# Kernel tuning notes

Measured on AMD Instinct MI355X. Metric: run time of the kernel, lower is better.

Reference implementation:

```python
import jax, jax.numpy as jnp
import numpy as np

ST_HIDDEN = 128
ST_HEADS = 4
ST_LAYERS = 3
RES_SCALE = 1.0
DK = ST_HIDDEN // ST_HEADS


def build_3d_adj(spatial_ei, spatial_ea, n_nodes, window):
    # replicate spatial edges per time slice with node offset t*n_nodes
    offs = (jnp.arange(window) * n_nodes)[None, :, None]  # [1,W,1]
    all_sp_idx = (spatial_ei[:, None, :] + offs).reshape(2, -1)  # [2, W*E]
    all_sp_attr = jnp.tile(spatial_ea, (window, 1))  # [W*E, De]
    # temporal edges t -> t+1 for every node
    src = jnp.arange((window - 1) * n_nodes)
    temp_idx = jnp.stack([src, src + n_nodes], axis=0)  # [2, (W-1)*N]
    temp_attr = jnp.broadcast_to(spatial_ea.mean(axis=0, keepdims=True),
                                 (temp_idx.shape[1], spatial_ea.shape[1]))
    ei = jnp.concatenate([all_sp_idx, temp_idx], axis=1)
    ea = jnp.concatenate([all_sp_attr, temp_attr], axis=0)
    return ei, ea


def seg_softmax(logits, dst, num_nodes):
    # logits [E,H], segment softmax over dst (pyg_softmax)
    m = jax.ops.segment_max(logits, dst, num_segments=num_nodes)  # [N,H]
    ex = jnp.exp(logits - m[dst])
    s = jax.ops.segment_sum(ex, dst, num_segments=num_nodes)
    return ex / (s[dst] + 1e-16)


def layernorm(x, g, b, eps=1e-5):
    mu = x.mean(-1, keepdims=True)
    var = ((x - mu) ** 2).mean(-1, keepdims=True)
    return (x - mu) * jax.lax.rsqrt(var + eps) * g + b


def block(x, ei, ea, qw, qb, kw, kb, vw, vb, fw, fb, ow, ob, ln_g, ln_b):
    B, Nt, _ = x.shape
    H, dk = ST_HEADS, DK
    Q = (x @ qw + qb).reshape(B, Nt, H, dk)
    K = (x @ kw + kb).reshape(B, Nt, H, dk)
    V = (x @ vw + vb).reshape(B, Nt, H, dk)
    src, dst = ei[0], ei[1]
    q_e = Q[:, dst]  # [B,E,H,dk]
    k_e = K[:, src]
    v_e = V[:, src]
    film = ea @ fw + fb  # [E, 2*hidden]
    gamma, beta = jnp.split(film, 2, axis=-1)
    gamma = gamma.reshape(1, -1, H, dk)
    beta = beta.reshape(1, -1, H, dk)
    k_e = k_e * (1.0 + gamma) + beta
    logits = (q_e * k_e).sum(-1) / np.sqrt(dk).astype(np.float32)  # [B,E,H]
    att = jax.vmap(lambda l: seg_softmax(l, dst, Nt))(logits)
    msg = att[..., None] * v_e  # [B,E,H,dk]
    out = jnp.zeros((B, Nt, H, dk), x.dtype).at[:, dst].add(msg)
    y = out.reshape(B, Nt, H * dk) @ ow + ob
    return layernorm(x + y, ln_g, ln_b)


def setup_inputs() -> dict:
    key = jax.random.key(0)
    ks = jax.random.split(key, 12)
    B, W, N, Fin, E, De = 2, 16, 1000, 16, 16000, 8
    H, L = ST_HIDDEN, ST_LAYERS
    g = lambda k, s: jax.random.normal(k, s, jnp.float32) * 0.05
    return {
        "xw": jax.random.normal(ks[0], (B, W, N, Fin), jnp.float32),
        "spatial_ei": jax.random.randint(ks[1], (2, E), 0, N),
        "spatial_ea": jax.random.normal(ks[2], (E, De), jnp.float32),
        "in_w": g(ks[3], (Fin, H)), "in_b": jnp.zeros((H,), jnp.float32),
        "qw": g(ks[4], (L, H, H)), "qb": jnp.zeros((L, H), jnp.float32),
        "kw": g(ks[5], (L, H, H)), "kb": jnp.zeros((L, H), jnp.float32),
        "vw": g(ks[6], (L, H, H)), "vb": jnp.zeros((L, H), jnp.float32),
        "fw": g(ks[7], (L, De, 2 * H)), "fb": jnp.zeros((L, 2 * H), jnp.float32),
        "ow": g(ks[8], (L, H, H)), "ob": jnp.zeros((L, H), jnp.float32),
        "ln_g": jnp.ones((L, H), jnp.float32), "ln_b": jnp.zeros((L, H), jnp.float32),
        "head_w": g(ks[9], (H, 1)), "head_b": jnp.zeros((1,), jnp.float32),
    }


def reference(xw, spatial_ei, spatial_ea, in_w, in_b, qw, qb, kw, kb, vw, vb,
              fw, fb, ow, ob, ln_g, ln_b, head_w, head_b):
    B, W, N, Fin = xw.shape
    ei, ea = build_3d_adj(spatial_ei, spatial_ea, N, W)
    x = xw.reshape(B, W * N, Fin) @ in_w + in_b
    for l in range(ST_LAYERS):
        bx = block(x, ei, ea, qw[l], qb[l], kw[l], kb[l], vw[l], vb[l],
                   fw[l], fb[l], ow[l], ob[l], ln_g[l], ln_b[l])
        x = x + RES_SCALE * (bx - x)
    last = x.reshape(B, W, N, -1)[:, -1]  # [B,N,H]
    return jax.nn.softplus(last @ head_w + head_b).squeeze(-1)  # [B,N]
```

## Files before the change

### kernel.cpp

```cpp
#include <hip/hip_runtime.h>
#include <math.h>

constexpr int B    = 2;
constexpr int W    = 16;
constexpr int N    = 1000;
constexpr int FIN  = 16;
constexpr int E    = 16000;
constexpr int DE   = 8;
constexpr int H    = 128;
constexpr int L    = 3;
constexpr int WL   = 4;
constexpr int W0G  = 12;
constexpr int RPB  = WL * N;
constexpr int ROWS = B * RPB;
constexpr int NMAT = 12;
constexpr int NFILM = (E + 1 + 7) / 8;

__device__ __forceinline__ float dot4(float4 a, float4 b) {
  return a.x * b.x + a.y * b.y + a.z * b.z + a.w * b.w;
}
__device__ __forceinline__ float dpp_add_xor1(float x) {
  int y = __builtin_amdgcn_update_dpp(0, __float_as_int(x), 0xB1, 0xF, 0xF, true);
  return x + __int_as_float(y);
}
__device__ __forceinline__ float dpp_add_xor2(float x) {
  int y = __builtin_amdgcn_update_dpp(0, __float_as_int(x), 0x4E, 0xF, 0xF, true);
  return x + __int_as_float(y);
}
__device__ __forceinline__ float headSum32(float p) {
  p = dpp_add_xor1(p);
  p = dpp_add_xor2(p);
  p += __shfl_xor(p, 4);
  p += __shfl_xor(p, 8);
  p += __shfl_xor(p, 16);
  return p;
}

__global__ void k_prep(const int* __restrict__ ei, const float* __restrict__ ea,
                       const float* __restrict__ qw, const float* __restrict__ kw,
                       const float* __restrict__ vw, const float* __restrict__ ow,
                       float4* __restrict__ wTp4,
                       const float* __restrict__ xw, const float* __restrict__ in_w,
                       const float* __restrict__ in_b, float* __restrict__ x,
                       float* __restrict__ meanea, int* __restrict__ offs,
                       int* __restrict__ cursor) {
  __shared__ union {
    struct { int cnt[1024]; int sT[256]; } sc;
    struct { float xwS[64][FIN]; float inS[FIN][H]; } ip;
    float sbuf[256];
  } sm;
  int bid = blockIdx.x;
  int t = threadIdx.x;
  if (bid == 0) {
    int* cnt = sm.sc.cnt;
    for (int i = t; i < 1024; i += 256) cnt[i] = 0;
    __syncthreads();
    for (int e0 = t; e0 < E; e0 += 1024) {
      int v[4];
      #pragma unroll
      for (int j = 0; j < 4; j++) {
        int e = e0 + j * 256;
        v[j] = (e < E) ? ei[E + e] : -1;
      }
      #pragma unroll
      for (int j = 0; j < 4; j++) if (v[j] >= 0) atomicAdd(&cnt[v[j]], 1);
    }
    __syncthreads();
    int idx0 = t * 4;
    int c0 = cnt[idx0], c1 = cnt[idx0 + 1], c2 = cnt[idx0 + 2], c3 = cnt[idx0 + 3];
    int run = c0 + c1 + c2 + c3;
    int* sT = sm.sc.sT;
    sT[t] = run;
    __syncthreads();
    for (int st = 1; st < 256; st <<= 1) {
      int add = (t >= st) ? sT[t - st] : 0;
      __syncthreads();
      sT[t] += add;
      __syncthreads();
    }
    int pos = sT[t] - run;
    int cs[4] = {c0, c1, c2, c3};
    #pragma unroll
    for (int j = 0; j < 4; j++) {
      int i = idx0 + j;
      if (i < N) { offs[i + 1] = pos + cs[j]; cursor[i] = pos; }
      pos += cs[j];
    }
    if (t == 0) offs[0] = 0;
  } else if (bid < 49) {
    int u0 = (bid - 1) * 1024;
    #pragma unroll
    for (int q = 0; q < 4; q++) {
      int o = u0 + q * 256 + t;
      int mat = o >> 12, rem = o & 4095;
      int kk4 = rem >> 7, c = rem & 127;
      int l = mat >> 2, mm = mat & 3;
      const float* src = ((mm == 0) ? qw : (mm == 1) ? kw : (mm == 2) ? vw : ow)
                         + (long)l * H * H;
      int k0 = kk4 * 4;
      float4 v4 = make_float4(src[(k0 + 0) * H + c], src[(k0 + 1) * H + c],
                              src[(k0 + 2) * H + c], src[(k0 + 3) * H + c]);
      wTp4[o] = v4;
    }
  } else if (bid < 81) {
    int eb = bid - 49;
    int d = t & 7, g = t >> 3;
    float s = 0.f;
    for (int e = eb * 32 + g; e < E; e += 32 * 32) s += ea[e * DE + d];
    sm.sbuf[t] = s;
    __syncthreads();
    for (int st = 16; st >= 1; st >>= 1) {
      if (g < st) sm.sbuf[g * 8 + d] += sm.sbuf[(g + st) * 8 + d];
      __syncthreads();
    }
    if (g == 0) atomicAdd(&meanea[d], sm.sbuf[d]);
  } else {
    int bi = bid - 81;
    int b = bi / 63, tt = bi % 63;
    int lr0 = tt * 64;
    for (int i = t; i < 64 * FIN; i += 256) {
      int r = i >> 4, k = i & 15;
      int lr = lr0 + r;
      float val = 0.f;
      if (lr < RPB) {
        int wl = lr / N, n = lr % N;
        val = xw[(((long)b * W + (W0G + wl)) * N + n) * FIN + k];
      }
      sm.ip.xwS[r][k] = val;
    }
    for (int i = t; i < FIN * H; i += 256) sm.ip.inS[i >> 7][i & 127] = in_w[i];
    __syncthreads();
    #pragma unroll
    for (int qi = 0; qi < 8; qi++) {
      int idx = t + qi * 256;
      int r = idx >> 5, cq = idx & 31;
      int lr = lr0 + r;
      if (lr < RPB) {
        float4 acc = *(const float4*)(in_b + cq * 4);
        #pragma unroll
        for (int k = 0; k < FIN; k++) {
          float xv = sm.ip.xwS[r][k];
          float4 w4 = *(const float4*)(&sm.ip.inS[k][cq * 4]);
          acc.x += xv * w4.x; acc.y += xv * w4.y; acc.z += xv * w4.z; acc.w += xv * w4.w;
        }
        *(float4*)(x + ((long)b * RPB + lr) * H + cq * 4) = acc;
      }
    }
  }
}

__global__ void k_mid(const float* __restrict__ X, const float4* __restrict__ wTp4,
                      int matBase,
                      const float* __restrict__ bq, const float* __restrict__ bk,
                      const float* __restrict__ bv,
                      float* __restrict__ Cq, float* __restrict__ KV,
                      int base, int rows_pb, int tiles, int nT,
                      const float* __restrict__ ea, const float* __restrict__ fwl,
                      const float* __restrict__ fbl, const float* __restrict__ meanea,
                      unsigned int* __restrict__ filmh,
                      const int* __restrict__ ei, int* __restrict__ cursor,
                      int2* __restrict__ csr) {
  __shared__ float xs[32][H];
  int u = blockIdx.x;
  int t = threadIdx.x;
  if (u < 2 * nT) {
    int role = u / nT;
    int r2 = u % nT;
    int bb = r2 / tiles, tt = r2 % tiles;
    int lr0 = tt * 32;
    long grow0 = (long)bb * RPB + base + lr0;
    #pragma unroll
    for (int qi = 0; qi < 4; qi++) {
      int idx = t + qi * 256;
      int r = idx >> 5, c4 = idx & 31;
      float4 v4 = make_float4(0.f, 0.f, 0.f, 0.f);
      if (lr0 + r < rows_pb) v4 = *(const float4*)(X + (grow0 + r) * H + c4 * 4);
      *(float4*)&xs[r][c4 * 4] = v4;
    }
    __syncthreads();
    int cg = t & 31, rg = t >> 5;
    if (role == 0) {
      const float4* wp = wTp4 + (long)(matBase + 0) * 32 * H;
      float4 bias4 = *(const float4*)(bq + cg * 4);
      float4 a0 = bias4, a1 = bias4, a2 = bias4, a3 = bias4;
      #pragma unroll 4
      for (int kk4 = 0; kk4 < 32; kk4++) {
        const float4* wr = wp + kk4 * H + cg * 4;
        float4 w0 = wr[0], w1 = wr[1], w2 = wr[2], w3 = wr[3];
        float4 x0 = *(const float4*)&xs[rg * 4 + 0][kk4 * 4];
        float4 x1 = *(const float4*)&xs[rg * 4 + 1][kk4 * 4];
        float4 x2 = *(const float4*)&xs[rg * 4 + 2][kk4 * 4];
        float4 x3 = *(const float4*)&xs[rg * 4 + 3][kk4 * 4];
        a0.x += dot4(x0, w0); a0.y += dot4(x0, w1); a0.z += dot4(x0, w2); a0.w += dot4(x0, w3);
        a1.x += dot4(x1, w0); a1.y += dot4(x1, w1); a1.z += dot4(x1, w2); a1.w += dot4(x1, w3);
        a2.x += dot4(x2, w0); a2.y += dot4(x2, w1); a2.z += dot4(x2, w2); a2.w += dot4(x2, w3);
        a3.x += dot4(x3, w0); a3.y += dot4(x3, w1); a3.z += dot4(x3, w2); a3.w += dot4(x3, w3);
      }
      int lrr = lr0 + rg * 4;
      if (lrr + 0 < rows_pb) *(float4*)(Cq + (grow0 + rg * 4 + 0) * H + cg * 4) = a0;
      if (lrr + 1 < rows_pb) *(float4*)(Cq + (grow0 + rg * 4 + 1) * H + cg * 4) = a1;
      if (lrr + 2 < rows_pb) *(float4*)(Cq + (grow0 + rg * 4 + 2) * H + cg * 4) = a2;
      if (lrr + 3 < rows_pb) *(float4*)(Cq + (grow0 + rg * 4 + 3) * H + cg * 4) = a3;
    } else {
      const float4* wpk = wTp4 + (long)(matBase + 1) * 32 * H;
      const float4* wpv = wTp4 + (long)(matBase + 2) * 32 * H;
      float4 bk4 = *(const float4*)(bk + cg * 4);
      float4 bv4 = *(const float4*)(bv + cg * 4);
      float4 k0 = bk4, k1 = bk4, k2 = bk4, k3 = bk4;
      float4 v0 = bv4, v1 = bv4, v2 = bv4, v3 = bv4;
      #pragma unroll 2
      for (int kk4 = 0; kk4 < 32; kk4++) {
        const float4* wrk = wpk + kk4 * H + cg * 4;
        const float4* wrv = wpv + kk4 * H + cg * 4;
        float4 wk0 = wrk[0], wk1 = wrk[1], wk2 = wrk[2], wk3 = wrk[3];
        float4 wv0 = wrv[0], wv1 = wrv[1], wv2 = wrv[2], wv3 = wrv[3];
        float4 x0 = *(const float4*)&xs[rg * 4 + 0][kk4 * 4];
        float4 x1 = *(const float4*)&xs[rg * 4 + 1][kk4 * 4];
        float4 x2 = *(const float4*)&xs[rg * 4 + 2][kk4 * 4];
        float4 x3 = *(const float4*)&xs[rg * 4 + 3][kk4 * 4];
        k0.x += dot4(x0, wk0); k0.y += dot4(x0, wk1); k0.z += dot4(x0, wk2); k0.w += dot4(x0, wk3);
        k1.x += dot4(x1, wk0); k1.y += dot4(x1, wk1); k1.z += dot4(x1, wk2); k1.w += dot4(x1, wk3);
        k2.x += dot4(x2, wk0); k2.y += dot4(x2, wk1); k2.z += dot4(x2, wk2); k2.w += dot4(x2, wk3);
        k3.x += dot4(x3, wk0); k3.y += dot4(x3, wk1); k3.z += dot4(x3, wk2); k3.w += dot4(x3, wk3);
        v0.x += dot4(x0, wv0); v0.y += dot4(x0, wv1); v0.z += dot4(x0, wv2); v0.w += dot4(x0, wv3);
        v1.x += dot4(x1, wv0); v1.y += dot4(x1, wv1); v1.z += dot4(x1, wv2); v1.w += dot4(x1, wv3);
        v2.x += dot4(x2, wv0); v2.y += dot4(x2, wv1); v2.z += dot4(x2, wv2); v2.w += dot4(x2, wv3);
        v3.x += dot4(x3, wv0); v3.y += dot4(x3, wv1); v3.z += dot4(x3, wv2); v3.w += dot4(x3, wv3);
      }
      int lrr = lr0 + rg * 4;
      float4 ks[4] = {k0, k1, k2, k3};
      float4 vs[4] = {v0, v1, v2, v3};
      #pragma unroll
      for (int i = 0; i < 4; i++) {
        if (lrr + i < rows_pb) {
          float* bp = KV + (grow0 + rg * 4 + i) * (2 * H) + cg * 8;
          *(float4*)bp       = make_float4(ks[i].x, vs[i].x, ks[i].y, vs[i].y);
          *(float4*)(bp + 4) = make_float4(ks[i].z, vs[i].z, ks[i].w, vs[i].w);
        }
      }
    }
  } else if (u < 2 * nT + NFILM) {
    int ru = u - 2 * nT;
    int c = t & 127, g2 = t >> 7;
    float rgw[DE], rbw[DE];
    #pragma unroll
    for (int d = 0; d < DE; d++) {
      rgw[d] = fwl[d * 2 * H + c];
      rbw[d] = fwl[d * 2 * H + H + c];
    }
    float fbg = fbl[c], fbb = fbl[H + c];
    int e0 = ru * 8 + g2 * 4;
    for (int e = e0; e < e0 + 4; e++) {
      if (e > E) break;
      float a[DE];
      if (e < E) {
        float4 a0 = *(const float4*)(ea + (long)e * DE);
        float4 a1 = *(const float4*)(ea + (long)e * DE + 4);
        a[0] = a0.x; a[1] = a0.y; a[2] = a0.z; a[3] = a0.w;
        a[4] = a1.x; a[5] = a1.y; a[6] = a1.z; a[7] = a1.w;
      } else {
        #pragma unroll
        for (int d = 0; d < DE; d++) a[d] = meanea[d] * (1.0f / E);
      }
      float g = fbg, be = fbb;
      #pragma unroll
      for (int d = 0; d < DE; d++) {
        g  += a[d] * rgw[d];
        be += a[d] * rbw[d];
      }
      unsigned int gb = __float_as_uint(g);
      gb = (gb + 0x7fffu + ((gb >> 16) & 1u)) >> 16;
      unsigned int bb_ = __float_as_uint(be);
      bb_ = (bb_ + 0x7fffu + ((bb_ >> 16) & 1u)) & 0xffff0000u;
      filmh[(long)e * H + c] = gb | bb_;
    }
  } else {
    int f = u - 2 * nT - NFILM;
    int e = f * 256 + t;
    if (e < E) {
      int src = ei[e];
      int dst = ei[E + e];
      int pos = atomicAdd(&cursor[dst], 1);
      csr[pos] = make_int2(src, e);
    }
  }
}

__global__ void k_attn_oln(const float* __restrict__ Qb, const float* __restrict__ KV,
                           const unsigned int* __restrict__ filmh,
                           const int* __restrict__ offs, const int2* __restrict__ csr,
                           const float* __restrict__ x, const float4* __restrict__ owp,
                           const float* __restrict__ ob, const float* __restrict__ lng,
                           const float* __restrict__ lnb, float* __restrict__ xo,
                           int out_lo,
                           const float* __restrict__ hw, const float* __restrict__ hb,
                           float* __restrict__ out, int do_head) {
  __shared__ float sab[2][H];
  __shared__ float red[2][2];
  int t = threadIdx.x;
  int half = t >> 7, tid = t & 127;
  int idx = blockIdx.x * 2 + half;
  int nwin = WL - out_lo;
  int b = idx / (nwin * N);
  int rem = idx % (nwin * N);
  int wl = out_lo + rem / N;
  int n = rem % N;
  long drow = ((long)b * WL + wl) * N + n;
  float q = Qb[drow * H + tid];
  long sbase = ((long)b * WL + wl) * N;
  long trow  = ((long)b * WL + wl - 1) * N + n;
  const float scale = 0.17677669529663687f;
  int i0 = offs[n], i1 = offs[n + 1];

  unsigned int fh = filmh[(long)E * H + tid];
  float g  = __uint_as_float(fh << 16);
  float be = __uint_as_float(fh & 0xffff0000u);
  float2 kvt = *(const float2*)(KV + trow * (2 * H) + tid * 2);
  float pp = q * (kvt.x * (1.f + g) + be);
  float pe = __expf(headSum32(pp) * scale);
  float ssum = pe, acc = pe * kvt.y;

  for (int i8 = i0; i8 < i1; i8 += 8) {
    #pragma unroll
    for (int j = 0; j < 8; j++) {
      int i = i8 + j;
      int ic = (i < i1) ? i : (i1 - 1);
      int2 se = csr[ic];
      long srow = sbase + se.x;
      unsigned int f2 = filmh[(long)se.y * H + tid];
      float g2 = __uint_as_float(f2 << 16);
      float b2 = __uint_as_float(f2 & 0xffff0000u);
      float2 kv2 = *(const float2*)(KV + srow * (2 * H) + tid * 2);
      float p2  = q * (kv2.x * (1.f + g2) + b2);
      float pe2 = __expf(headSum32(p2) * scale);
      pe2 = (i < i1) ? pe2 : 0.f;
      ssum += pe2;
      acc  += pe2 * kv2.y;
    }
  }
  float ab = acc / (ssum + 1e-16f);

  sab[half][tid] = ab;
  __syncthreads();
  float y = ob[tid];
  #pragma unroll 8
  for (int kk4 = 0; kk4 < 32; kk4++) {
    float4 w4 = owp[kk4 * H + tid];
    float4 a4 = *(const float4*)&sab[half][kk4 * 4];
    y += dot4(a4, w4);
  }

  float s = x[drow * H + tid] + y;
  float r1 = s;
  #pragma unroll
  for (int off = 32; off >= 1; off >>= 1) r1 += __shfl_xor(r1, off);
  {
    int w = (t >> 6) & 1;
    __syncthreads();
    if ((t & 63) == 0) red[half][w] = r1;
    __syncthreads();
  }
  float mu = (red[half][0] + red[half][1]) * (1.f / H);
  float dv = s - mu;
  float r2v = dv * dv;
  #pragma unroll
  for (int off = 32; off >= 1; off >>= 1) r2v += __shfl_xor(r2v, off);
  {
    int w = (t >> 6) & 1;
    __syncthreads();
    if ((t & 63) == 0) red[half][w] = r2v;
    __syncthreads();
  }
  float var = (red[half][0] + red[half][1]) * (1.f / H);
  float o = dv * rsqrtf(var + 1e-5f) * lng[tid] + lnb[tid];

  if (!do_head) {
    xo[drow * H + tid] = o;
  } else {
    float hv = o * hw[tid];
    float r3 = hv;
    #pragma unroll
    for (int off = 32; off >= 1; off >>= 1) r3 += __shfl_xor(r3, off);
    int w = (t >> 6) & 1;
    __syncthreads();
    if ((t & 63) == 0) red[half][w] = r3;
    __syncthreads();
    if (tid == 0) {
      float z = red[half][0] + red[half][1] + hb[0];
      out[b * N + n] = fmaxf(z, 0.f) + log1pf(expf(-fabsf(z)));
    }
  }
}

extern "C" void kernel_launch(void* const* d_in, const int* in_sizes, int n_in,
                              void* d_out, int out_size, void* d_ws, size_t ws_size,
                              hipStream_t stream) {
  const float* xw   = (const float*)d_in[0];
  const int*   ei   = (const int*)d_in[1];
  const float* ea   = (const float*)d_in[2];
  const float* in_w = (const float*)d_in[3];
  const float* in_b = (const float*)d_in[4];
  const float* qw   = (const float*)d_in[5];
  const float* qb   = (const float*)d_in[6];
  const float* kw   = (const float*)d_in[7];
  const float* kb   = (const float*)d_in[8];
  const float* vw   = (const float*)d_in[9];
  const float* vb   = (const float*)d_in[10];
  const float* fw   = (const float*)d_in[11];
  const float* fb   = (const float*)d_in[12];
  const float* ow   = (const float*)d_in[13];
  const float* ob   = (const float*)d_in[14];
  const float* ln_g = (const float*)d_in[15];
  const float* ln_b = (const float*)d_in[16];
  const float* hw   = (const float*)d_in[17];
  const float* hb   = (const float*)d_in[18];
  float* out = (float*)d_out;

  float* ws   = (float*)d_ws;
  float* x    = ws;
  float* x2   = x  + (long)ROWS * H;
  float* Qb   = x2 + (long)ROWS * H;
  float* KVb  = Qb + (long)ROWS * H;
  float* wTp  = KVb + (long)ROWS * 2 * H;
  unsigned int* filmh = (unsigned int*)(wTp + (long)NMAT * H * H);
  float* meanea = (float*)(filmh + (long)(E + 1) * H);
  int* offs    = (int*)(meanea + 8);
  int* cursor  = offs + N + 1;
  int2* csr    = (int2*)(cursor + N);
  float4* wTp4 = (float4*)wTp;

  hipMemsetAsync(meanea, 0, 8 * sizeof(float), stream);
  k_prep<<<207, 256, 0, stream>>>(ei, ea, qw, kw, vw, ow, wTp4,
                                  xw, in_w, in_b, x, meanea, offs, cursor);

  float* xa = x;
  float* xb = x2;
  for (int l = 0; l < L; l++) {
    int out_lo = l + 1;
    int rows_pb = (WL - l) * N;
    int tiles = (rows_pb + 31) / 32;
    int nT = B * tiles;
    int nFill = (l == 0) ? (E + 255) / 256 : 0;
    int nMid = 2 * nT + NFILM + nFill;
    k_mid<<<nMid, 256, 0, stream>>>(
        xa, wTp4, l * 4, qb + (long)l * H, kb + (long)l * H, vb + (long)l * H,
        Qb, KVb, l * N, rows_pb, tiles, nT,
        ea, fw + (long)l * DE * 2 * H, fb + (long)l * 2 * H, meanea, filmh,
        ei, cursor, csr);
    int nout = B * (WL - out_lo) * N;
    int last = (l == L - 1) ? 1 : 0;
    k_attn_oln<<<nout / 2, 256, 0, stream>>>(
        Qb, KVb, filmh, offs, csr,
        xa, wTp4 + ((long)l * 4 + 3) * 32 * H, ob + (long)l * H,
        ln_g + (long)l * H, ln_b + (long)l * H, xb, out_lo,
        hw, hb, out, last);
    float* tmp = xa; xa = xb; xb = tmp;
  }
}
```

Baseline: 273.7 us.

## Pack K/V as bf16, CSR-order FiLM, build CSR in prep, trim Q rows

K and V projections are now stored as packed bf16 pairs in one 32-bit word, which halves the gather traffic in the attention kernel. The CSR fill moves from the first k_mid launch into k_prep's single scan block. FiLM values are now written in CSR order, so the attention loop reads them contiguously by edge position rather than through the edge id. Q is computed only for the rows that produce outputs, and the edge loop unroll drops from 8 to 4. The bf16 K/V adds rounding error, and serialising the CSR fill in one block may lengthen k_prep.

```diff
diff --git a/kernel.cpp b/kernel.cpp
--- a/kernel.cpp
+++ b/kernel.cpp
@@ -35,6 +35,14 @@
   p += __shfl_xor(p, 16);
   return p;
 }
+__device__ __forceinline__ unsigned int bf16lo(float f) {
+  unsigned int u = __float_as_uint(f);
+  return (u + 0x7fffu + ((u >> 16) & 1u)) >> 16;
+}
+__device__ __forceinline__ unsigned int bf16hi(float f) {
+  unsigned int u = __float_as_uint(f);
+  return (u + 0x7fffu + ((u >> 16) & 1u)) & 0xffff0000u;
+}
 
 __global__ void k_prep(const int* __restrict__ ei, const float* __restrict__ ea,
                        const float* __restrict__ qw, const float* __restrict__ kw,
@@ -43,7 +51,7 @@
                        const float* __restrict__ xw, const float* __restrict__ in_w,
                        const float* __restrict__ in_b, float* __restrict__ x,
                        float* __restrict__ meanea, int* __restrict__ offs,
-                       int* __restrict__ cursor) {
+                       int2* __restrict__ csr) {
   __shared__ union {
     struct { int cnt[1024]; int sT[256]; } sc;
     struct { float xwS[64][FIN]; float inS[FIN][H]; } ip;
@@ -80,13 +88,27 @@
     }
     int pos = sT[t] - run;
     int cs[4] = {c0, c1, c2, c3};
+    __syncthreads();
     #pragma unroll
     for (int j = 0; j < 4; j++) {
       int i = idx0 + j;
-      if (i < N) { offs[i + 1] = pos + cs[j]; cursor[i] = pos; }
+      if (i < N) { offs[i + 1] = pos + cs[j]; cnt[i] = pos; }
       pos += cs[j];
     }
     if (t == 0) offs[0] = 0;
+    __syncthreads();
+    for (int e0 = t; e0 < E; e0 += 512) {
+      int d0 = ei[E + e0], s0 = ei[e0];
+      int e1 = e0 + 256;
+      int d1 = (e1 < E) ? ei[E + e1] : -1;
+      int s1 = (e1 < E) ? ei[e1] : 0;
+      int p0 = atomicAdd(&cnt[d0], 1);
+      csr[p0] = make_int2(s0, e0);
+      if (d1 >= 0) {
+        int p1 = atomicAdd(&cnt[d1], 1);
+        csr[p1] = make_int2(s1, e1);
+      }
+    }
   } else if (bid < 49) {
     int u0 = (bid - 1) * 1024;
     #pragma unroll
@@ -153,20 +175,23 @@
                       int matBase,
                       const float* __restrict__ bq, const float* __restrict__ bk,
                       const float* __restrict__ bv,
-                      float* __restrict__ Cq, float* __restrict__ KV,
-                      int base, int rows_pb, int tiles, int nT,
+                      float* __restrict__ Cq, unsigned int* __restrict__ KVu,
+                      int baseQ, int rowsQ, int tilesQ,
+                      int baseKV, int rowsKV, int tilesKV,
                       const float* __restrict__ ea, const float* __restrict__ fwl,
                       const float* __restrict__ fbl, const float* __restrict__ meanea,
-                      unsigned int* __restrict__ filmh,
-                      const int* __restrict__ ei, int* __restrict__ cursor,
-                      int2* __restrict__ csr) {
+                      unsigned int* __restrict__ filmh, const int2* __restrict__ csr) {
   __shared__ float xs[32][H];
   int u = blockIdx.x;
   int t = threadIdx.x;
-  if (u < 2 * nT) {
-    int role = u / nT;
-    int r2 = u % nT;
-    int bb = r2 / tiles, tt = r2 % tiles;
+  int nQ = B * tilesQ, nKV = B * tilesKV;
+  if (u < nQ + nKV) {
+    int role = (u < nQ) ? 0 : 1;
+    int r2   = (role == 0) ? u : (u - nQ);
+    int tls  = (role == 0) ? tilesQ : tilesKV;
+    int base = (role == 0) ? baseQ : baseKV;
+    int rows = (role == 0) ? rowsQ : rowsKV;
+    int bb = r2 / tls, tt = r2 % tls;
     int lr0 = tt * 32;
     long grow0 = (long)bb * RPB + base + lr0;
     #pragma unroll
@@ -174,7 +199,7 @@
       int idx = t + qi * 256;
       int r = idx >> 5, c4 = idx & 31;
       float4 v4 = make_float4(0.f, 0.f, 0.f, 0.f);
-      if (lr0 + r < rows_pb) v4 = *(const float4*)(X + (grow0 + r) * H + c4 * 4);
+      if (lr0 + r < rows) v4 = *(const float4*)(X + (grow0 + r) * H + c4 * 4);
       *(float4*)&xs[r][c4 * 4] = v4;
     }
     __syncthreads();
@@ -197,10 +222,10 @@
         a3.x += dot4(x3, w0); a3.y += dot4(x3, w1); a3.z += dot4(x3, w2); a3.w += dot4(x3, w3);
       }
       int lrr = lr0 + rg * 4;
-      if (lrr + 0 < rows_pb) *(float4*)(Cq + (grow0 + rg * 4 + 0) * H + cg * 4) = a0;
-      if (lrr + 1 < rows_pb) *(float4*)(Cq + (grow0 + rg * 4 + 1) * H + cg * 4) = a1;
-      if (lrr + 2 < rows_pb) *(float4*)(Cq + (grow0 + rg * 4 + 2) * H + cg * 4) = a2;
-      if (lrr + 3 < rows_pb) *(float4*)(Cq + (grow0 + rg * 4 + 3) * H + cg * 4) = a3;
+      if (lrr + 0 < rowsQ) *(float4*)(Cq + (grow0 + rg * 4 + 0) * H + cg * 4) = a0;
+      if (lrr + 1 < rowsQ) *(float4*)(Cq + (grow0 + rg * 4 + 1) * H + cg * 4) = a1;
+      if (lrr + 2 < rowsQ) *(float4*)(Cq + (grow0 + rg * 4 + 2) * H + cg * 4) = a2;
+      if (lrr + 3 < rowsQ) *(float4*)(Cq + (grow0 + rg * 4 + 3) * H + cg * 4) = a3;
     } else {
       const float4* wpk = wTp4 + (long)(matBase + 1) * 32 * H;
       const float4* wpv = wTp4 + (long)(matBase + 2) * 32 * H;
@@ -232,15 +257,18 @@
       float4 vs[4] = {v0, v1, v2, v3};
       #pragma unroll
       for (int i = 0; i < 4; i++) {
-        if (lrr + i < rows_pb) {
-          float* bp = KV + (grow0 + rg * 4 + i) * (2 * H) + cg * 8;
-          *(float4*)bp       = make_float4(ks[i].x, vs[i].x, ks[i].y, vs[i].y);
-          *(float4*)(bp + 4) = make_float4(ks[i].z, vs[i].z, ks[i].w, vs[i].w);
+        if (lrr + i < rowsKV) {
+          uint4 pk;
+          pk.x = bf16lo(ks[i].x) | bf16hi(vs[i].x);
+          pk.y = bf16lo(ks[i].y) | bf16hi(vs[i].y);
+          pk.z = bf16lo(ks[i].z) | bf16hi(vs[i].z);
+          pk.w = bf16lo(ks[i].w) | bf16hi(vs[i].w);
+          *(uint4*)(KVu + (grow0 + rg * 4 + i) * H + cg * 4) = pk;
         }
       }
     }
-  } else if (u < 2 * nT + NFILM) {
-    int ru = u - 2 * nT;
+  } else {
+    int ru = u - nQ - nKV;
     int c = t & 127, g2 = t >> 7;
     float rgw[DE], rbw[DE];
     #pragma unroll
@@ -254,8 +282,9 @@
       if (e > E) break;
       float a[DE];
       if (e < E) {
-        float4 a0 = *(const float4*)(ea + (long)e * DE);
-        float4 a1 = *(const float4*)(ea + (long)e * DE + 4);
+        int eid = csr[e].y;
+        float4 a0 = *(const float4*)(ea + (long)eid * DE);
+        float4 a1 = *(const float4*)(ea + (long)eid * DE + 4);
         a[0] = a0.x; a[1] = a0.y; a[2] = a0.z; a[3] = a0.w;
         a[4] = a1.x; a[5] = a1.y; a[6] = a1.z; a[7] = a1.w;
       } else {
@@ -268,25 +297,12 @@
         g  += a[d] * rgw[d];
         be += a[d] * rbw[d];
       }
-      unsigned int gb = __float_as_uint(g);
-      gb = (gb + 0x7fffu + ((gb >> 16) & 1u)) >> 16;
-      unsigned int bb_ = __float_as_uint(be);
-      bb_ = (bb_ + 0x7fffu + ((bb_ >> 16) & 1u)) & 0xffff0000u;
-      filmh[(long)e * H + c] = gb | bb_;
-    }
-  } else {
-    int f = u - 2 * nT - NFILM;
-    int e = f * 256 + t;
-    if (e < E) {
-      int src = ei[e];
-      int dst = ei[E + e];
-      int pos = atomicAdd(&cursor[dst], 1);
-      csr[pos] = make_int2(src, e);
-    }
-  }
-}
-
-__global__ void k_attn_oln(const float* __restrict__ Qb, const float* __restrict__ KV,
+      filmh[(long)e * H + c] = bf16lo(g) | bf16hi(be);
+    }
+  }
+}
+
+__global__ void k_attn_oln(const float* __restrict__ Qb, const unsigned int* __restrict__ KVu,
                            const unsigned int* __restrict__ filmh,
                            const int* __restrict__ offs, const int2* __restrict__ csr,
                            const float* __restrict__ x, const float4* __restrict__ owp,
@@ -315,27 +331,31 @@
   unsigned int fh = filmh[(long)E * H + tid];
   float g  = __uint_as_float(fh << 16);
   float be = __uint_as_float(fh & 0xffff0000u);
-  float2 kvt = *(const float2*)(KV + trow * (2 * H) + tid * 2);
-  float pp = q * (kvt.x * (1.f + g) + be);
+  unsigned int kvu = KVu[trow * H + tid];
+  float kv = __uint_as_float(kvu << 16);
+  float vv = __uint_as_float(kvu & 0xffff0000u);
+  float pp = q * (kv * (1.f + g) + be);
   float pe = __expf(headSum32(pp) * scale);
-  float ssum = pe, acc = pe * kvt.y;
-
-  for (int i8 = i0; i8 < i1; i8 += 8) {
-    #pragma unroll
-    for (int j = 0; j < 8; j++) {
-      int i = i8 + j;
+  float ssum = pe, acc = pe * vv;
+
+  for (int i4 = i0; i4 < i1; i4 += 4) {
+    #pragma unroll
+    for (int j = 0; j < 4; j++) {
+      int i = i4 + j;
       int ic = (i < i1) ? i : (i1 - 1);
       int2 se = csr[ic];
       long srow = sbase + se.x;
-      unsigned int f2 = filmh[(long)se.y * H + tid];
+      unsigned int f2 = filmh[(long)ic * H + tid];
       float g2 = __uint_as_float(f2 << 16);
       float b2 = __uint_as_float(f2 & 0xffff0000u);
-      float2 kv2 = *(const float2*)(KV + srow * (2 * H) + tid * 2);
-      float p2  = q * (kv2.x * (1.f + g2) + b2);
+      unsigned int kv2u = KVu[srow * H + tid];
+      float kv2 = __uint_as_float(kv2u << 16);
+      float vv2 = __uint_as_float(kv2u & 0xffff0000u);
+      float p2  = q * (kv2 * (1.f + g2) + b2);
       float pe2 = __expf(headSum32(p2) * scale);
       pe2 = (i < i1) ? pe2 : 0.f;
       ssum += pe2;
-      acc  += pe2 * kv2.y;
+      acc  += pe2 * vv2;
     }
   }
   float ab = acc / (ssum + 1e-16f);
@@ -420,37 +440,37 @@
   float* x    = ws;
   float* x2   = x  + (long)ROWS * H;
   float* Qb   = x2 + (long)ROWS * H;
-  float* KVb  = Qb + (long)ROWS * H;
-  float* wTp  = KVb + (long)ROWS * 2 * H;
+  unsigned int* KVu = (unsigned int*)(Qb + (long)ROWS * H);
+  float* wTp  = (float*)(KVu + (long)ROWS * H);
   unsigned int* filmh = (unsigned int*)(wTp + (long)NMAT * H * H);
   float* meanea = (float*)(filmh + (long)(E + 1) * H);
   int* offs    = (int*)(meanea + 8);
-  int* cursor  = offs + N + 1;
-  int2* csr    = (int2*)(cursor + N);
+  int2* csr    = (int2*)(offs + N + 2);
   float4* wTp4 = (float4*)wTp;
 
   hipMemsetAsync(meanea, 0, 8 * sizeof(float), stream);
   k_prep<<<207, 256, 0, stream>>>(ei, ea, qw, kw, vw, ow, wTp4,
-                                  xw, in_w, in_b, x, meanea, offs, cursor);
+                                  xw, in_w, in_b, x, meanea, offs, csr);
 
   float* xa = x;
   float* xb = x2;
   for (int l = 0; l < L; l++) {
     int out_lo = l + 1;
-    int rows_pb = (WL - l) * N;
-    int tiles = (rows_pb + 31) / 32;
-    int nT = B * tiles;
-    int nFill = (l == 0) ? (E + 255) / 256 : 0;
-    int nMid = 2 * nT + NFILM + nFill;
+    int rowsQ  = (WL - l - 1) * N;
+    int rowsKV = (WL - l) * N;
+    int tilesQ  = (rowsQ + 31) / 32;
+    int tilesKV = (rowsKV + 31) / 32;
+    int nMid = B * tilesQ + B * tilesKV + NFILM;
     k_mid<<<nMid, 256, 0, stream>>>(
         xa, wTp4, l * 4, qb + (long)l * H, kb + (long)l * H, vb + (long)l * H,
-        Qb, KVb, l * N, rows_pb, tiles, nT,
-        ea, fw + (long)l * DE * 2 * H, fb + (long)l * 2 * H, meanea, filmh,
-        ei, cursor, csr);
+        Qb, KVu,
+        (l + 1) * N, rowsQ, tilesQ,
+        l * N, rowsKV, tilesKV,
+        ea, fw + (long)l * DE * 2 * H, fb + (long)l * 2 * H, meanea, filmh, csr);
     int nout = B * (WL - out_lo) * N;
     int last = (l == L - 1) ? 1 : 0;
     k_attn_oln<<<nout / 2, 256, 0, stream>>>(
-        Qb, KVb, filmh, offs, csr,
+        Qb, KVu, filmh, offs, csr,
         xa, wTp4 + ((long)l * 4 + 3) * 32 * H, ob + (long)l * H,
         ln_g + (long)l * H, ln_b + (long)l * H, xb, out_lo,
         hw, hb, out, last);
```

Result: no change. 276.9 us (+1.2%).
